# Performance work log

Measured on AMD Instinct MI355X. Metric: run time of the kernel, lower is better.

## Reference

```python
import jax, jax.numpy as jnp
import numpy as np

N_NODES = 20000
N_EDGES = 640000
F_IN = 128
HID = 128


def setup_inputs() -> dict:
    key = jax.random.key(0)
    ks = jax.random.split(key, 12)
    d = {}
    d["x"] = jax.random.normal(ks[0], (N_NODES, F_IN), dtype=jnp.float32)
    d["edge_index"] = jax.random.randint(ks[1], (2, N_EDGES), 0, N_NODES, dtype=jnp.int64)
    d["edge_weight"] = jax.random.uniform(ks[2], (N_EDGES,), dtype=jnp.float32)
    d["h"] = jax.random.normal(ks[3], (N_NODES, HID), dtype=jnp.float32)
    s1 = 1.0 / np.sqrt(F_IN)
    s2 = 1.0 / np.sqrt(HID)
    s3 = 1.0 / np.sqrt(2 * HID)
    d["W1"] = jax.random.uniform(ks[4], (F_IN, HID), jnp.float32, -s1, s1)
    d["b1"] = jnp.zeros((HID,), jnp.float32)
    d["W2"] = jax.random.uniform(ks[5], (HID, HID), jnp.float32, -s2, s2)
    d["b2"] = jnp.zeros((HID,), jnp.float32)
    d["Wu"] = jax.random.uniform(ks[6], (2 * HID, HID), jnp.float32, -s3, s3)
    d["bu"] = jax.random.uniform(ks[7], (HID,), jnp.float32, -s3, s3)
    d["Wr"] = jax.random.uniform(ks[8], (2 * HID, HID), jnp.float32, -s3, s3)
    d["br"] = jax.random.uniform(ks[9], (HID,), jnp.float32, -s3, s3)
    d["Wc"] = jax.random.uniform(ks[10], (2 * HID, HID), jnp.float32, -s3, s3)
    d["bc"] = jax.random.uniform(ks[11], (HID,), jnp.float32, -s3, s3)
    return d


def _gcn_layer(x, W, b, src, dst, norm, n):
    # GCNConv: transform then normalized scatter-add aggregation
    xw = x @ W                                    # [N, out]
    agg = jax.ops.segment_sum(xw[src] * norm[:, None], dst, num_segments=n)
    return agg + b


def reference(x, edge_index, edge_weight, h, W1, b1, W2, b2, Wu, bu, Wr, br, Wc, bc):
    n = x.shape[0]
    loops = jnp.arange(n, dtype=edge_index.dtype)
    src = jnp.concatenate([edge_index[0], loops])
    dst = jnp.concatenate([edge_index[1], loops])
    ew = jnp.concatenate([edge_weight, jnp.ones((n,), edge_weight.dtype)])
    # symmetric GCN normalization with self-loops
    deg = jax.ops.segment_sum(ew, dst, num_segments=n)
    dinv = jnp.where(deg > 0, jax.lax.rsqrt(deg), 0.0)
    norm = dinv[src] * ew * dinv[dst]             # [E+N]
    # 2-layer GCN: in->hid (ReLU) -> hid->hid
    h1 = jax.nn.relu(_gcn_layer(x, W1, b1, src, dst, norm, n))
    g = _gcn_layer(h1, W2, b2, src, dst, norm, n)
    xg = jax.nn.sigmoid(g)                        # [N, HID]
    # GRU-style gating
    xh = jnp.concatenate([xg, h], axis=-1)        # [N, 2*HID]
    u = jax.nn.sigmoid(xh @ Wu + bu)
    r = jax.nn.sigmoid(xh @ Wr + br)
    c = jnp.tanh(jnp.concatenate([xg, r * h], axis=-1) @ Wc + bc)
    return u * h + (1.0 - u) * c
```

## Files before the change

kernel.cpp:

```cpp
#include <hip/hip_runtime.h>
#include <math.h>

#define N_NODES 20000
#define N_EDGES 640000
#define HID 128
#define NPAD 20224
#define NBLK 79
#define NSHARD 8

typedef __attribute__((ext_vector_type(8))) short bf16x8;
typedef __attribute__((ext_vector_type(4))) float f32x4;
typedef __attribute__((ext_vector_type(2))) float f32x2;

#define FIX_SCALE 274877906944.0
#define FIX_MASK ((1ull << 48) - 1)

__device__ inline short f2bf(float f) {
    unsigned u = __builtin_bit_cast(unsigned, f);
    u += 0x7fffu + ((u >> 16) & 1u);
    return (short)(u >> 16);
}
__device__ inline float bf2f(short s) {
    unsigned u = ((unsigned)(unsigned short)s) << 16;
    return __builtin_bit_cast(float, u);
}
__device__ inline uint2 pack_bf4(float4 f) {
    uint2 v;
    v.x = (unsigned)(unsigned short)f2bf(f.x) | ((unsigned)(unsigned short)f2bf(f.y) << 16);
    v.y = (unsigned)(unsigned short)f2bf(f.z) | ((unsigned)(unsigned short)f2bf(f.w) << 16);
    return v;
}
__device__ inline bf16x8 cvt8(float4 a0, float4 a1) {
    bf16x8 v;
    v[0] = f2bf(a0.x); v[1] = f2bf(a0.y); v[2] = f2bf(a0.z); v[3] = f2bf(a0.w);
    v[4] = f2bf(a1.x); v[5] = f2bf(a1.y); v[6] = f2bf(a1.z); v[7] = f2bf(a1.w);
    return v;
}
__device__ inline unsigned char f2fp8(float f) {
    return (unsigned char)(__builtin_amdgcn_cvt_pk_fp8_f32(f, f, 0, false) & 0xff);
}
__device__ inline float4 unpack_fp8x4(unsigned v) {
    f32x2 lo = __builtin_amdgcn_cvt_pk_f32_fp8((int)v, false);
    f32x2 hi = __builtin_amdgcn_cvt_pk_f32_fp8((int)v, true);
    return make_float4(lo[0], lo[1], hi[0], hi[1]);
}

__device__ inline float4 agg_node(int node, int half, int l,
                                  const unsigned char* __restrict__ xw,
                                  const int* __restrict__ rp,
                                  const int2* __restrict__ csr,
                                  const float* __restrict__ dinv) {
    float4 acc = {0.f, 0.f, 0.f, 0.f};
    if (half == 0) {
        float dv = dinv[node];
        float dv2 = dv * dv;
        float4 v = unpack_fp8x4(((const unsigned*)(xw + (size_t)node * HID))[l]);
        acc.x = v.x * dv2; acc.y = v.y * dv2; acc.z = v.z * dv2; acc.w = v.w * dv2;
    }
    int j = rp[node], end = rp[node + 1];
    for (; j + 15 < end; j += 16) {
        int2 e[8];
#pragma unroll
        for (int i = 0; i < 8; i++) e[i] = csr[j + 2 * i + half];
        unsigned v[8];
#pragma unroll
        for (int i = 0; i < 8; i++) v[i] = ((const unsigned*)(xw + (size_t)e[i].x * HID))[l];
#pragma unroll
        for (int i = 0; i < 8; i++) {
            float w = __builtin_bit_cast(float, e[i].y);
            float4 f = unpack_fp8x4(v[i]);
            acc.x += f.x * w; acc.y += f.y * w; acc.z += f.z * w; acc.w += f.w * w;
        }
    }
    for (; j + 7 < end; j += 8) {
        int2 e[4];
#pragma unroll
        for (int i = 0; i < 4; i++) e[i] = csr[j + 2 * i + half];
        unsigned v[4];
#pragma unroll
        for (int i = 0; i < 4; i++) v[i] = ((const unsigned*)(xw + (size_t)e[i].x * HID))[l];
#pragma unroll
        for (int i = 0; i < 4; i++) {
            float w = __builtin_bit_cast(float, e[i].y);
            float4 f = unpack_fp8x4(v[i]);
            acc.x += f.x * w; acc.y += f.y * w; acc.z += f.z * w; acc.w += f.w * w;
        }
    }
    for (; j + 1 < end; j += 2) {
        int2 e0 = csr[j + half];
        float4 f = unpack_fp8x4(((const unsigned*)(xw + (size_t)e0.x * HID))[l]);
        float w0 = __builtin_bit_cast(float, e0.y);
        acc.x += f.x * w0; acc.y += f.y * w0; acc.z += f.z * w0; acc.w += f.w * w0;
    }
    if (j < end && half == 0) {
        int2 e0 = csr[j];
        float4 f = unpack_fp8x4(((const unsigned*)(xw + (size_t)e0.x * HID))[l]);
        float w0 = __builtin_bit_cast(float, e0.y);
        acc.x += f.x * w0; acc.y += f.y * w0; acc.z += f.z * w0; acc.w += f.w * w0;
    }
    acc.x += __shfl_xor(acc.x, 32);
    acc.y += __shfl_xor(acc.y, 32);
    acc.z += __shfl_xor(acc.z, 32);
    acc.w += __shfl_xor(acc.w, 32);
    return acc;
}

__global__ __launch_bounds__(256) void k_prep(const float* __restrict__ W1, const float* __restrict__ W2,
                                              const float* __restrict__ Wu, const float* __restrict__ Wr,
                                              const float* __restrict__ Wc,
                                              short* WT1, short* WT2, short* WTu, short* WTr, short* WTc,
                                              unsigned long long* packed) {
    int b = blockIdx.x;
    int tid = threadIdx.x;
    if (b < 512) {
        int i = b * 256 + tid;
        if (i < 32768) {
            const float* W = (i < 16384) ? W1 : W2;
            short* T = (i < 16384) ? WT1 : WT2;
            int j = i & 16383;
            int n = j >> 7, k = j & 127;
            T[n * 128 + k] = f2bf(W[k * 128 + n]);
        } else {
            int j = i - 32768;
            const float* W = Wu; short* T = WTu;
            if (j >= 65536)      { W = Wc; T = WTc; j -= 65536; }
            else if (j >= 32768) { W = Wr; T = WTr; j -= 32768; }
            int n = j >> 8, k = j & 255;
            T[n * 256 + k] = f2bf(W[k * 128 + n]);
        }
    } else {
        int i = (b - 512) * 256 + tid;
        if (i < NSHARD * NPAD) packed[i] = 0ull;
    }
}

__global__ __launch_bounds__(256) void k_hist_gemm(unsigned long long* packed, int* __restrict__ rank,
                                                   const int* __restrict__ dst,
                                                   const float* __restrict__ ew,
                                                   const float* __restrict__ x,
                                                   const short* __restrict__ WT1,
                                                   unsigned char* __restrict__ xw) {
    __shared__ short As[16 * 136];
    int tid = threadIdx.x;
    if (blockIdx.x < 2500) {
        int e = blockIdx.x * 256 + tid;
        int shard = blockIdx.x & (NSHARD - 1);
        int d = dst[e];
        unsigned long long add = (1ull << 48) | (unsigned long long)((double)ew[e] * FIX_SCALE);
        unsigned long long old = atomicAdd(&packed[shard * NPAD + d], add);
        rank[e] = (int)(old >> 48);
        return;
    }
    int r0 = (blockIdx.x - 2500) * 16;
    {
        int row = tid >> 4;
        int col0 = (tid & 15) * 8;
        const float* p = x + (size_t)(r0 + row) * HID + col0;
        *(bf16x8*)(&As[row * 136 + col0]) = cvt8(*(const float4*)p, *(const float4*)(p + 4));
    }
    __syncthreads();
    int wave = tid >> 6, lane = tid & 63;
    int m = lane & 15, quad = lane >> 4;
    f32x4 acc[2];
    acc[0] = (f32x4){0.f, 0.f, 0.f, 0.f};
    acc[1] = acc[0];
#pragma unroll
    for (int ks = 0; ks < 4; ks++) {
        int k0 = ks * 32 + quad * 8;
        bf16x8 a = *(const bf16x8*)(&As[m * 136 + k0]);
#pragma unroll
        for (int j = 0; j < 2; j++) {
            int n = (wave * 2 + j) * 16 + m;
            bf16x8 b = *(const bf16x8*)(WT1 + n * 128 + k0);
            acc[j] = __builtin_amdgcn_mfma_f32_16x16x32_bf16(a, b, acc[j], 0, 0, 0);
        }
    }
#pragma unroll
    for (int j = 0; j < 2; j++) {
        int col = (wave * 2 + j) * 16 + m;
#pragma unroll
        for (int rg = 0; rg < 4; rg++) {
            int grow = r0 + quad * 4 + rg;
            xw[(size_t)grow * HID + col] = f2fp8(acc[j][rg]);
        }
    }
}

__global__ __launch_bounds__(256) void k_scan_part(const unsigned long long* __restrict__ packed,
                                                   int* __restrict__ tot, int* __restrict__ bsum) {
    __shared__ int red[256];
    int tid = threadIdx.x;
    int i = blockIdx.x * 256 + tid;
    int t = 0;
    if (i < N_NODES) {
#pragma unroll
        for (int s = 0; s < NSHARD; s++) t += (int)(packed[s * NPAD + i] >> 48);
        tot[i] = t;
    }
    red[tid] = t;
    __syncthreads();
    for (int off = 128; off > 0; off >>= 1) {
        if (tid < off) red[tid] += red[tid + off];
        __syncthreads();
    }
    if (tid == 0) bsum[blockIdx.x] = red[0];
}

__global__ __launch_bounds__(256) void k_scan_final(const unsigned long long* __restrict__ packed,
                                                    const int* __restrict__ tot,
                                                    const int* __restrict__ bsum,
                                                    int* __restrict__ rp, int* __restrict__ sb,
                                                    float* __restrict__ dinv) {
    __shared__ int smem[256];
    __shared__ int red[256];
    int tid = threadIdx.x;
    red[tid] = (tid < blockIdx.x) ? bsum[tid] : 0;
    int i = blockIdx.x * 256 + tid;
    int t = (i < N_NODES) ? tot[i] : 0;
    smem[tid] = t;
    __syncthreads();
    for (int off = 128; off > 0; off >>= 1) {
        if (tid < off) red[tid] += red[tid + off];
        __syncthreads();
    }
    for (int off = 1; off < 256; off <<= 1) {
        int x = (tid >= off) ? smem[tid - off] : 0;
        __syncthreads();
        smem[tid] += x;
        __syncthreads();
    }
    if (i < N_NODES) {
        int excl = smem[tid] - t + red[0];
        rp[i] = excl;
        if (i == N_NODES - 1) rp[N_NODES] = excl + t;
        int acc = excl;
        double deg = 1.0;
#pragma unroll
        for (int s = 0; s < NSHARD; s++) {
            unsigned long long p = packed[s * NPAD + i];
            sb[s * NPAD + i] = acc;
            acc += (int)(p >> 48);
            deg += (double)(p & FIX_MASK) * (1.0 / FIX_SCALE);
        }
        dinv[i] = rsqrtf((float)deg);
    }
}

__global__ __launch_bounds__(256) void k_fill(const int* __restrict__ src,
                                              const int* __restrict__ dst,
                                              const float* __restrict__ ew,
                                              const float* __restrict__ dinv,
                                              const int* __restrict__ sb,
                                              const int* __restrict__ rank,
                                              int2* __restrict__ csr) {
    int e = blockIdx.x * 256 + threadIdx.x;
    int shard = blockIdx.x & (NSHARD - 1);
    if (e < N_EDGES) {
        int s = src[e], d = dst[e];
        int slot = sb[shard * NPAD + d] + rank[e];
        float w = dinv[s] * ew[e] * dinv[d];
        csr[slot] = make_int2(s, __builtin_bit_cast(int, w));
    }
}

__global__ __launch_bounds__(256) void k_agg(const unsigned char* __restrict__ xw,
                                             short* __restrict__ outb,
                                             const int* __restrict__ rp,
                                             const int2* __restrict__ csr,
                                             const float* __restrict__ dinv,
                                             const float* __restrict__ bias,
                                             int act) {
    int node = blockIdx.x * 4 + (threadIdx.x >> 6);
    int lane = threadIdx.x & 63;
    int half = lane >> 5, l = lane & 31;
    float4 acc = agg_node(node, half, l, xw, rp, csr, dinv);
    if (half == 0) {
        float4 b = ((const float4*)bias)[l];
        acc.x += b.x; acc.y += b.y; acc.z += b.z; acc.w += b.w;
        if (act == 0) {
            acc.x = fmaxf(acc.x, 0.f); acc.y = fmaxf(acc.y, 0.f);
            acc.z = fmaxf(acc.z, 0.f); acc.w = fmaxf(acc.w, 0.f);
        } else {
            acc.x = 1.f / (1.f + __expf(-acc.x)); acc.y = 1.f / (1.f + __expf(-acc.y));
            acc.z = 1.f / (1.f + __expf(-acc.z)); acc.w = 1.f / (1.f + __expf(-acc.w));
        }
        ((uint2*)(outb + (size_t)node * HID))[l] = pack_bf4(acc);
    }
}

__global__ __launch_bounds__(256) void k_gemm2(const short* __restrict__ Ab,
                                               const short* __restrict__ WT,
                                               unsigned char* __restrict__ Cb) {
    __shared__ short As[16 * 136];
    int tid = threadIdx.x;
    int r0 = blockIdx.x * 16;
    {
        int row = tid >> 4;
        int col0 = (tid & 15) * 8;
        *(bf16x8*)(&As[row * 136 + col0]) = *(const bf16x8*)(Ab + (size_t)(r0 + row) * HID + col0);
    }
    __syncthreads();
    int wave = tid >> 6, lane = tid & 63;
    int m = lane & 15, quad = lane >> 4;
    f32x4 acc[2];
    acc[0] = (f32x4){0.f, 0.f, 0.f, 0.f};
    acc[1] = acc[0];
#pragma unroll
    for (int ks = 0; ks < 4; ks++) {
        int k0 = ks * 32 + quad * 8;
        bf16x8 a = *(const bf16x8*)(&As[m * 136 + k0]);
#pragma unroll
        for (int j = 0; j < 2; j++) {
            int n = (wave * 2 + j) * 16 + m;
            bf16x8 b = *(const bf16x8*)(WT + n * 128 + k0);
            acc[j] = __builtin_amdgcn_mfma_f32_16x16x32_bf16(a, b, acc[j], 0, 0, 0);
        }
    }
#pragma unroll
    for (int j = 0; j < 2; j++) {
        int col = (wave * 2 + j) * 16 + m;
#pragma unroll
        for (int rg = 0; rg < 4; rg++) {
            int grow = r0 + quad * 4 + rg;
            Cb[(size_t)grow * HID + col] = f2fp8(acc[j][rg]);
        }
    }
}

__global__ __launch_bounds__(256) void k_gate(const short* __restrict__ xgb,
                                              const float* __restrict__ hf,
                                              const short* __restrict__ WTu, const short* __restrict__ WTr,
                                              const short* __restrict__ WTc,
                                              const float* __restrict__ pbu, const float* __restrict__ pbr,
                                              const float* __restrict__ pbc,
                                              float* __restrict__ out) {
    __shared__ short Xs[16 * 264];
    int tid = threadIdx.x;
    int r0 = blockIdx.x * 16;
#pragma unroll
    for (int i = 0; i < 2; i++) {
        int c = tid + i * 256;
        int row = c >> 5;
        int col0 = (c & 31) * 8;
        int grow = r0 + row;
        bf16x8 v;
        if (col0 < 128) {
            v = *(const bf16x8*)(xgb + (size_t)grow * HID + col0);
        } else {
            const float* p = hf + (size_t)grow * HID + (col0 - 128);
            v = cvt8(*(const float4*)p, *(const float4*)(p + 4));
        }
        *(bf16x8*)(&Xs[row * 264 + col0]) = v;
    }
    __syncthreads();
    int wave = tid >> 6, lane = tid & 63;
    int m = lane & 15, quad = lane >> 4;
    f32x4 au[2], ar[2];
    au[0] = (f32x4){0.f, 0.f, 0.f, 0.f};
    au[1] = au[0]; ar[0] = au[0]; ar[1] = au[0];
#pragma unroll
    for (int ks = 0; ks < 8; ks++) {
        int k0 = ks * 32 + quad * 8;
        bf16x8 a = *(const bf16x8*)(&Xs[m * 264 + k0]);
#pragma unroll
        for (int j = 0; j < 2; j++) {
            int n = (wave * 2 + j) * 16 + m;
            bf16x8 bu_f = *(const bf16x8*)(WTu + n * 256 + k0);
            au[j] = __builtin_amdgcn_mfma_f32_16x16x32_bf16(a, bu_f, au[j], 0, 0, 0);
            bf16x8 br_f = *(const bf16x8*)(WTr + n * 256 + k0);
            ar[j] = __builtin_amdgcn_mfma_f32_16x16x32_bf16(a, br_f, ar[j], 0, 0, 0);
        }
    }
    __syncthreads();
#pragma unroll
    for (int j = 0; j < 2; j++) {
        int col = (wave * 2 + j) * 16 + m;
        float brv = pbr[col];
#pragma unroll
        for (int rg = 0; rg < 4; rg++) {
            int trow = quad * 4 + rg;
            float rv = 1.f / (1.f + __expf(-(ar[j][rg] + brv)));
            float hv = bf2f(Xs[trow * 264 + 128 + col]);
            Xs[trow * 264 + 128 + col] = f2bf(rv * hv);
        }
    }
    __syncthreads();
    f32x4 ac[2];
    ac[0] = (f32x4){0.f, 0.f, 0.f, 0.f};
    ac[1] = ac[0];
#pragma unroll
    for (int ks = 0; ks < 8; ks++) {
        int k0 = ks * 32 + quad * 8;
        bf16x8 a = *(const bf16x8*)(&Xs[m * 264 + k0]);
#pragma unroll
        for (int j = 0; j < 2; j++) {
            int n = (wave * 2 + j) * 16 + m;
            bf16x8 bc_f = *(const bf16x8*)(WTc + n * 256 + k0);
            ac[j] = __builtin_amdgcn_mfma_f32_16x16x32_bf16(a, bc_f, ac[j], 0, 0, 0);
        }
    }
#pragma unroll
    for (int j = 0; j < 2; j++) {
        int col = (wave * 2 + j) * 16 + m;
        float buv = pbu[col], bcv = pbc[col];
#pragma unroll
        for (int rg = 0; rg < 4; rg++) {
            int grow = r0 + quad * 4 + rg;
            float uv = 1.f / (1.f + __expf(-(au[j][rg] + buv)));
            float cv = tanhf(ac[j][rg] + bcv);
            float hv = hf[(size_t)grow * HID + col];
            out[(size_t)grow * HID + col] = uv * hv + (1.f - uv) * cv;
        }
    }
}

extern "C" void kernel_launch(void* const* d_in, const int* in_sizes, int n_in,
                              void* d_out, int out_size, void* d_ws, size_t ws_size,
                              hipStream_t stream) {
    const float* x  = (const float*)d_in[0];
    const int*   ei = (const int*)d_in[1];
    const float* ew = (const float*)d_in[2];
    const float* h  = (const float*)d_in[3];
    const float* W1 = (const float*)d_in[4];
    const float* b1 = (const float*)d_in[5];
    const float* W2 = (const float*)d_in[6];
    const float* b2 = (const float*)d_in[7];
    const float* Wu = (const float*)d_in[8];
    const float* bu = (const float*)d_in[9];
    const float* Wr = (const float*)d_in[10];
    const float* br = (const float*)d_in[11];
    const float* Wc = (const float*)d_in[12];
    const float* bc = (const float*)d_in[13];
    const int* src = ei;
    const int* dst = ei + N_EDGES;
    float* out = (float*)d_out;

    const size_t NH = (size_t)N_NODES * HID;
    float* ws = (float*)d_ws;
    float* dinv = ws;
    int*   rp   = (int*)(ws + NPAD);
    unsigned long long* packed = (unsigned long long*)(ws + 2 * NPAD);
    int*   sb   = (int*)(ws + 18 * NPAD);
    int*   tot  = (int*)(ws + 26 * NPAD);
    int*   bsum = (int*)(ws + 27 * NPAD);
    int*   rank = (int*)(ws + 27 * NPAD + 128);
    int2*  csr  = (int2*)(ws + 27 * NPAD + 128 + N_EDGES);
    unsigned char* xw  = (unsigned char*)(ws + 27 * NPAD + 128 + 3 * N_EDGES);
    unsigned char* xw2 = xw + NH;
    short* h1b = (short*)(xw2 + NH);
    short* xgb = h1b + NH;
    short* WT1 = xgb + NH;
    short* WT2 = WT1 + 16384;
    short* WTu = WT2 + 16384;
    short* WTr = WTu + 32768;
    short* WTc = WTr + 32768;

    k_prep<<<512 + (NSHARD * NPAD + 255) / 256, 256, 0, stream>>>(
        W1, W2, Wu, Wr, Wc, WT1, WT2, WTu, WTr, WTc, packed);
    k_hist_gemm<<<2500 + N_NODES / 16, 256, 0, stream>>>(packed, rank, dst, ew, x, WT1, xw);
    k_scan_part<<<NBLK, 256, 0, stream>>>(packed, tot, bsum);
    k_scan_final<<<NBLK, 256, 0, stream>>>(packed, tot, bsum, rp, sb, dinv);
    k_fill<<<N_EDGES / 256, 256, 0, stream>>>(src, dst, ew, dinv, sb, rank, csr);
    k_agg<<<N_NODES / 4, 256, 0, stream>>>(xw, h1b, rp, csr, dinv, b1, 0);
    k_gemm2<<<N_NODES / 16, 256, 0, stream>>>(h1b, WT2, xw2);
    k_agg<<<N_NODES / 4, 256, 0, stream>>>(xw2, xgb, rp, csr, dinv, b2, 1);
    k_gate<<<N_NODES / 16, 256, 0, stream>>>(xgb, h, WTu, WTr, WTc, bu, br, bc, out);
}
```

Before: 230.0 us.

## Double histogram shards, add 32-edge aggregation unroll, tile weight transpose

Raises the number of atomic histogram shards from 8 to 16 to cut contention on per-node degree atomics, and moves workspace offsets to fit the larger packed buffer. Adds a 32-edge unrolled gather loop in the aggregation so more loads are in flight per iteration. Rewrites the weight transpose/bf16 conversion to use an LDS tile with vectorized loads and stores instead of strided scalar accesses. The extra shards mean more zeroing and more work in the scans, and the wider unroll raises register pressure.

```diff
diff --git a/kernel.cpp b/kernel.cpp
--- a/kernel.cpp
+++ b/kernel.cpp
@@ -6,7 +6,7 @@
 #define HID 128
 #define NPAD 20224
 #define NBLK 79
-#define NSHARD 8
+#define NSHARD 16
 
 typedef __attribute__((ext_vector_type(8))) short bf16x8;
 typedef __attribute__((ext_vector_type(4))) float f32x4;
@@ -58,6 +58,20 @@
         acc.x = v.x * dv2; acc.y = v.y * dv2; acc.z = v.z * dv2; acc.w = v.w * dv2;
     }
     int j = rp[node], end = rp[node + 1];
+    for (; j + 31 < end; j += 32) {
+        int2 e[16];
+#pragma unroll
+        for (int i = 0; i < 16; i++) e[i] = csr[j + 2 * i + half];
+        unsigned v[16];
+#pragma unroll
+        for (int i = 0; i < 16; i++) v[i] = ((const unsigned*)(xw + (size_t)e[i].x * HID))[l];
+#pragma unroll
+        for (int i = 0; i < 16; i++) {
+            float w = __builtin_bit_cast(float, e[i].y);
+            float4 f = unpack_fp8x4(v[i]);
+            acc.x += f.x * w; acc.y += f.y * w; acc.z += f.z * w; acc.w += f.w * w;
+        }
+    }
     for (; j + 15 < end; j += 16) {
         int2 e[8];
 #pragma unroll
@@ -110,26 +124,40 @@
                                               const float* __restrict__ Wc,
                                               short* WT1, short* WT2, short* WTu, short* WTr, short* WTc,
                                               unsigned long long* packed) {
+    __shared__ short tile[64][66];
     int b = blockIdx.x;
     int tid = threadIdx.x;
-    if (b < 512) {
-        int i = b * 256 + tid;
-        if (i < 32768) {
-            const float* W = (i < 16384) ? W1 : W2;
-            short* T = (i < 16384) ? WT1 : WT2;
-            int j = i & 16383;
-            int n = j >> 7, k = j & 127;
-            T[n * 128 + k] = f2bf(W[k * 128 + n]);
+    if (b < 32) {
+        const float* W; short* T; int K, kt, nt;
+        if (b < 8) {
+            W = (b < 4) ? W1 : W2; T = (b < 4) ? WT1 : WT2; K = 128;
+            int t = b & 3; kt = t >> 1; nt = t & 1;
         } else {
-            int j = i - 32768;
-            const float* W = Wu; short* T = WTu;
-            if (j >= 65536)      { W = Wc; T = WTc; j -= 65536; }
-            else if (j >= 32768) { W = Wr; T = WTr; j -= 32768; }
-            int n = j >> 8, k = j & 255;
-            T[n * 256 + k] = f2bf(W[k * 128 + n]);
+            int j = b - 8; int mat = j >> 3;
+            W = mat == 0 ? Wu : (mat == 1 ? Wr : Wc);
+            T = mat == 0 ? WTu : (mat == 1 ? WTr : WTc);
+            K = 256;
+            int t = j & 7; kt = t >> 1; nt = t & 1;
+        }
+        int r = tid >> 2, q = tid & 3;
+        {
+            const float* p = W + (size_t)(kt * 64 + r) * 128 + nt * 64 + q * 16;
+            float4 a0 = ((const float4*)p)[0], a1 = ((const float4*)p)[1];
+            float4 a2 = ((const float4*)p)[2], a3 = ((const float4*)p)[3];
+            *(bf16x8*)(&tile[r][q * 16])     = cvt8(a0, a1);
+            *(bf16x8*)(&tile[r][q * 16 + 8]) = cvt8(a2, a3);
+        }
+        __syncthreads();
+        {
+            bf16x8 v0, v1;
+#pragma unroll
+            for (int i = 0; i < 8; i++) { v0[i] = tile[q * 16 + i][r]; v1[i] = tile[q * 16 + 8 + i][r]; }
+            short* d = T + (size_t)(nt * 64 + r) * K + kt * 64 + q * 16;
+            *(bf16x8*)d = v0;
+            *(bf16x8*)(d + 8) = v1;
         }
     } else {
-        int i = (b - 512) * 256 + tid;
+        int i = (b - 32) * 256 + tid;
         if (i < NSHARD * NPAD) packed[i] = 0ull;
     }
 }
@@ -440,12 +468,12 @@
     float* dinv = ws;
     int*   rp   = (int*)(ws + NPAD);
     unsigned long long* packed = (unsigned long long*)(ws + 2 * NPAD);
-    int*   sb   = (int*)(ws + 18 * NPAD);
-    int*   tot  = (int*)(ws + 26 * NPAD);
-    int*   bsum = (int*)(ws + 27 * NPAD);
-    int*   rank = (int*)(ws + 27 * NPAD + 128);
-    int2*  csr  = (int2*)(ws + 27 * NPAD + 128 + N_EDGES);
-    unsigned char* xw  = (unsigned char*)(ws + 27 * NPAD + 128 + 3 * N_EDGES);
+    int*   sb   = (int*)(ws + 34 * NPAD);
+    int*   tot  = (int*)(ws + 50 * NPAD);
+    int*   bsum = (int*)(ws + 51 * NPAD);
+    int*   rank = (int*)(ws + 51 * NPAD + 128);
+    int2*  csr  = (int2*)(ws + 51 * NPAD + 128 + N_EDGES);
+    unsigned char* xw  = (unsigned char*)(ws + 51 * NPAD + 128 + 3 * N_EDGES);
     unsigned char* xw2 = xw + NH;
     short* h1b = (short*)(xw2 + NH);
     short* xgb = h1b + NH;
@@ -455,7 +483,7 @@
     short* WTr = WTu + 32768;
     short* WTc = WTr + 32768;
 
-    k_prep<<<512 + (NSHARD * NPAD + 255) / 256, 256, 0, stream>>>(
+    k_prep<<<32 + (NSHARD * NPAD + 255) / 256, 256, 0, stream>>>(
         W1, W2, Wu, Wr, Wc, WT1, WT2, WTu, WTr, WTc, packed);
     k_hist_gemm<<<2500 + N_NODES / 16, 256, 0, stream>>>(packed, rank, dst, ew, x, WT1, xw);
     k_scan_part<<<NBLK, 256, 0, stream>>>(packed, tot, bsum);
```

Result: slower. 235.0 us (+2.2%).
